# Kernel tuning notes

Hardware: AMD Instinct MI355X
Metric: run time of the kernel (lower is better)

Reference implementation:

```python
import jax, jax.numpy as jnp
import numpy as np

DIM, DIM_KQ, DIM_V, N = 1024, 64, 64, 8192

def setup_inputs() -> dict:
    key = jax.random.key(0)
    kx, kq, kk, kv = jax.random.split(key, 4)
    x = jax.random.normal(kx, (N, DIM), dtype=jnp.float32)
    # original uses torch.rand (uniform [0,1)) for parameter init
    w_q = jax.random.uniform(kq, (DIM, DIM_KQ), dtype=jnp.float32)
    w_k = jax.random.uniform(kk, (DIM, DIM_KQ), dtype=jnp.float32)
    w_v = jax.random.uniform(kv, (DIM, DIM_V), dtype=jnp.float32)
    return {"x": x, "w_q": w_q, "w_k": w_k, "w_v": w_v}

def reference(x, w_q, w_k, w_v):
    q = x @ w_q            # [N, dkq]
    k = x @ w_k            # [N, dkq]
    v = x @ w_v            # [N, dv]
    scale = 1.0 / jnp.sqrt(jnp.asarray(DIM_KQ, dtype=x.dtype))
    att_s = (q @ k.T) * scale           # [N, N]
    att_w = jax.nn.softmax(att_s, axis=-1)
    return att_w @ v                    # [N, dv]
```

## Files before the change

### kernel.cpp

```cpp
#include <hip/hip_runtime.h>
#include <hip/hip_bf16.h>
#include <math.h>

constexpr int N    = 8192;
constexpr int DIM  = 1024;

typedef __attribute__((ext_vector_type(8))) short bf16x8;
typedef __attribute__((ext_vector_type(4))) float f32x4;

__device__ inline unsigned short f2bf(float f) {
    unsigned u = __float_as_uint(f);
    u += 0x7fffu + ((u >> 16) & 1u);
    return (unsigned short)(u >> 16);
}
__device__ inline float bf2f(unsigned short h) {
    return __uint_as_float((unsigned)h << 16);
}
__device__ inline unsigned cvtpk(float a, float b) {
    unsigned r;
    asm("v_cvt_pk_bf16_f32 %0, %1, %2" : "=v"(r) : "v"(a), "v"(b));
    return r;
}
__device__ inline void gload16(const void* gsrc, void* ldst) {
    typedef __attribute__((address_space(1))) const unsigned int GU;
    typedef __attribute__((address_space(3))) unsigned int LU;
    __builtin_amdgcn_global_load_lds((GU*)gsrc, (LU*)ldst, 16, 0, 0);
}

__global__ __launch_bounds__(256) void prep_w_kernel(
    const float* __restrict__ wq, const float* __restrict__ wk,
    const float* __restrict__ wv,
    unsigned short* __restrict__ wthi, unsigned short* __restrict__ wtlo)
{
    int idx = blockIdx.x * 256 + threadIdx.x;
    int c   = idx >> 10;
    int k   = idx & 1023;
    const float* wsrc = (c < 64) ? wq : (c < 128) ? wk : wv;
    float f = wsrc[(size_t)k * 64 + (c & 63)];
    unsigned short h = f2bf(f);
    int pos = c * 1024 + (k & ~63) + ((((k >> 3) & 7) ^ (c & 7)) << 3) + (k & 7);
    wthi[pos] = h;
    wtlo[pos] = f2bf(f - bf2f(h));
}

__global__ __launch_bounds__(256) void proj_kernel(
    const float* __restrict__ x,
    const unsigned short* __restrict__ wthi,
    const unsigned short* __restrict__ wtlo,
    unsigned short* __restrict__ qhi, unsigned short* __restrict__ qlo,
    unsigned short* __restrict__ khi, unsigned short* __restrict__ klo,
    unsigned short* __restrict__ vthi)
{
    __shared__ unsigned short As[2][2][4096];
    __shared__ unsigned short Bs[2][2][3072];

    const int tid  = threadIdx.x;
    const int lane = tid & 63;
    const int w    = tid >> 6;
    const int g16  = lane >> 4;
    const int i16  = lane & 15;
    const int row0 = blockIdx.x * 64;
    const int col0 = blockIdx.y * 48;

    float4 xn[2][4];
    auto loadX = [&](int t, int s) {
#pragma unroll
        for (int i = 0; i < 4; ++i) {
            int f4 = i * 256 + tid;
            xn[s][i] = *reinterpret_cast<const float4*>(
                x + (size_t)(row0 + (f4 >> 4)) * DIM + t * 64 + (f4 & 15) * 4);
        }
    };
    auto stageB = [&](int t, int buf) {
#pragma unroll
        for (int i = 0; i < 3; ++i) {
            int idx = i * 256 + tid;
            int p   = (idx >= 384) ? 1 : 0;
            int li  = idx - p * 384;
            const unsigned short* base = p ? wtlo : wthi;
            const unsigned short* src  = base + (size_t)(col0 + (li >> 3)) * 1024
                                         + t * 64 + (li & 7) * 8;
            gload16(src, (char*)&Bs[buf][p][0] + (size_t)li * 16);
        }
    };
    auto writeA = [&](int buf, int s) {
#pragma unroll
        for (int i = 0; i < 4; ++i) {
            int f4 = i * 256 + tid;
            int r = f4 >> 4, c4 = f4 & 15;
            float4 v = xn[s][i];
            unsigned h01 = cvtpk(v.x, v.y);
            unsigned h23 = cvtpk(v.z, v.w);
            float hx = __uint_as_float(h01 << 16);
            float hy = __uint_as_float(h01 & 0xffff0000u);
            float hz = __uint_as_float(h23 << 16);
            float hw = __uint_as_float(h23 & 0xffff0000u);
            uint2 uh = { h01, h23 };
            uint2 ul = { cvtpk(v.x - hx, v.y - hy), cvtpk(v.z - hz, v.w - hw) };
            int byte = r * 128 + (((c4 >> 1) ^ (r & 7)) << 4) + ((c4 & 1) << 3);
            *reinterpret_cast<uint2*>((char*)&As[buf][0][0] + byte) = uh;
            *reinterpret_cast<uint2*>((char*)&As[buf][1][0] + byte) = ul;
        }
    };

    f32x4 acc[3];
    acc[0] = acc[1] = acc[2] = (f32x4){0.f, 0.f, 0.f, 0.f};

    loadX(0, 0);
    loadX(1, 1);
    stageB(0, 0);
    writeA(0, 0);

    const int arow = w * 16 + i16;
#pragma unroll
    for (int t = 0; t < 16; ++t) {
        const int b = t & 1;
        __syncthreads();
        if (t < 15) stageB(t + 1, b ^ 1);
        if (t < 14) loadX(t + 2, b);
        bf16x8 ah[2], al[2];
#pragma unroll
        for (int kc = 0; kc < 2; ++kc) {
            int off = arow * 128 + ((((kc << 2) | g16) ^ (arow & 7)) << 4);
            ah[kc] = *reinterpret_cast<const bf16x8*>((char*)&As[b][0][0] + off);
            al[kc] = *reinterpret_cast<const bf16x8*>((char*)&As[b][1][0] + off);
        }
#pragma unroll
        for (int ct = 0; ct < 3; ++ct) {
            const int colL = ct * 16 + i16;
#pragma unroll
            for (int kc = 0; kc < 2; ++kc) {
                int off = colL * 128 + ((((kc << 2) | g16) ^ (colL & 7)) << 4);
                bf16x8 bh = *reinterpret_cast<const bf16x8*>((char*)&Bs[b][0][0] + off);
                bf16x8 bl = *reinterpret_cast<const bf16x8*>((char*)&Bs[b][1][0] + off);
                acc[ct] = __builtin_amdgcn_mfma_f32_16x16x32_bf16(ah[kc], bh, acc[ct], 0, 0, 0);
                acc[ct] = __builtin_amdgcn_mfma_f32_16x16x32_bf16(ah[kc], bl, acc[ct], 0, 0, 0);
                acc[ct] = __builtin_amdgcn_mfma_f32_16x16x32_bf16(al[kc], bh, acc[ct], 0, 0, 0);
            }
        }
        if (t < 15) writeA(b ^ 1, b ^ 1);
    }

    const float QSCALE = 0.180336880f;
#pragma unroll
    for (int ct = 0; ct < 3; ++ct) {
        int cglob = col0 + ct * 16 + i16;
        int g = cglob >> 6, c64 = cglob & 63;
#pragma unroll
        for (int rr = 0; rr < 4; ++rr) {
            int row = row0 + w * 16 + 4 * g16 + rr;
            float f = acc[ct][rr];
            if (g == 0) {
                f *= QSCALE;
                unsigned short h = f2bf(f);
                qhi[(size_t)row * 64 + c64] = h;
                qlo[(size_t)row * 64 + c64] = f2bf(f - bf2f(h));
            } else if (g == 1) {
                int ci = c64 ^ ((row & 7) << 3);
                unsigned short h = f2bf(f);
                khi[(size_t)row * 64 + ci] = h;
                klo[(size_t)row * 64 + ci] = f2bf(f - bf2f(h));
            } else {
                int cg  = row >> 3;
                int cgs = (cg & ~7) | ((cg & 7) ^ (c64 & 7));
                vthi[(size_t)c64 * 8192 + cgs * 8 + (row & 7)] = f2bf(f);
            }
        }
    }
}

constexpr int BQ = 128;
constexpr int BK = 64;

__global__ __launch_bounds__(256) void attn_kernel(
    const unsigned short* __restrict__ qhi, const unsigned short* __restrict__ qlo,
    const unsigned short* __restrict__ khi, const unsigned short* __restrict__ klo,
    const unsigned short* __restrict__ vthi,
    float* __restrict__ po, float* __restrict__ pm, float* __restrict__ pl,
    int keys_per_split)
{
    __shared__ __align__(16) unsigned short stage[2][12288];
    __shared__ __align__(16) unsigned short plds[4][2][1024];

    const int tid  = threadIdx.x;
    const int lane = tid & 63;
    const int w    = tid >> 6;
    const int g16  = lane >> 4;
    const int i16  = lane & 15;
    const int qrow0 = blockIdx.x * BQ;
    const int split = blockIdx.y;
    const int key0  = split * keys_per_split;
    const int nt    = keys_per_split / BK;
    const int xorm  = (i16 & 7) << 4;
    const int wbase = i16 * 128;

    bf16x8 qh[2][2], ql[2][2];
#pragma unroll
    for (int s = 0; s < 2; ++s) {
        const size_t qr = (size_t)(qrow0 + w * 32 + s * 16 + i16) * 64;
#pragma unroll
        for (int c = 0; c < 2; ++c) {
            qh[s][c] = *reinterpret_cast<const bf16x8*>(qhi + qr + c * 32 + g16 * 8);
            ql[s][c] = *reinterpret_cast<const bf16x8*>(qlo + qr + c * 32 + g16 * 8);
        }
    }
    bf16x8 ones;
#pragma unroll
    for (int e = 0; e < 8; ++e) ones[e] = (short)0x3F80;

    float m[2] = {-INFINITY, -INFINITY};
    f32x4 o_acc[2][4], o5[2];
#pragma unroll
    for (int s = 0; s < 2; ++s) {
        o5[s] = {0.f, 0.f, 0.f, 0.f};
#pragma unroll
        for (int db = 0; db < 4; ++db) o_acc[s][db] = {0.f, 0.f, 0.f, 0.f};
    }

    auto stageKV = [&](int t, int buf) {
        const int key0t = key0 + t * BK;
#pragma unroll
        for (int u = 0; u < 6; ++u) {
            int row = ((u & 1) << 5) + (tid >> 3);
            int ch  = tid & 7;
            const unsigned short* src;
            if (u < 2)      src = khi  + (size_t)(key0t + row) * 64 + ch * 8;
            else if (u < 4) src = klo  + (size_t)(key0t + row) * 64 + ch * 8;
            else            src = vthi + (size_t)row * 8192 + key0t + ch * 8;
            gload16(src, (char*)&stage[buf][0] + u * 4096 + tid * 16);
        }
    };

    stageKV(0, 0);

    for (int t = 0; t < nt; ++t) {
        const int b = t & 1;
        __syncthreads();
        if (t + 1 < nt) stageKV(t + 1, b ^ 1);
        const char* stg = (const char*)&stage[b][0];

        f32x4 sacc[2][4];
#pragma unroll
        for (int j = 0; j < 4; ++j) {
            sacc[0][j] = {0.f, 0.f, 0.f, 0.f};
            sacc[1][j] = {0.f, 0.f, 0.f, 0.f};
            const int kr = 16 * j + i16;
#pragma unroll
            for (int c = 0; c < 2; ++c) {
                const int byteO = kr * 128 + ((c * 64 + g16 * 16) ^ ((kr & 7) << 4));
                bf16x8 kh = *reinterpret_cast<const bf16x8*>(stg + byteO);
                bf16x8 kl = *reinterpret_cast<const bf16x8*>(stg + byteO + 8192);
#pragma unroll
                for (int s = 0; s < 2; ++s) {
                    sacc[s][j] = __builtin_amdgcn_mfma_f32_16x16x32_bf16(kh, qh[s][c], sacc[s][j], 0, 0, 0);
                    sacc[s][j] = __builtin_amdgcn_mfma_f32_16x16x32_bf16(kh, ql[s][c], sacc[s][j], 0, 0, 0);
                    sacc[s][j] = __builtin_amdgcn_mfma_f32_16x16x32_bf16(kl, qh[s][c], sacc[s][j], 0, 0, 0);
                }
            }
        }

        float aloc[2];
#pragma unroll
        for (int s = 0; s < 2; ++s) {
            float a0 = fmaxf(fmaxf(sacc[s][0][0], sacc[s][0][1]), fmaxf(sacc[s][0][2], sacc[s][0][3]));
            float a1 = fmaxf(fmaxf(sacc[s][1][0], sacc[s][1][1]), fmaxf(sacc[s][1][2], sacc[s][1][3]));
            float a2 = fmaxf(fmaxf(sacc[s][2][0], sacc[s][2][1]), fmaxf(sacc[s][2][2], sacc[s][2][3]));
            float a3 = fmaxf(fmaxf(sacc[s][3][0], sacc[s][3][1]), fmaxf(sacc[s][3][2], sacc[s][3][3]));
            aloc[s] = fmaxf(fmaxf(a0, a1), fmaxf(a2, a3));
        }
        int need = (aloc[0] > m[0] + 8.f) | (aloc[1] > m[1] + 8.f);
        if (__any(need)) {
#pragma unroll
            for (int s = 0; s < 2; ++s) {
                float x2 = fmaxf(aloc[s], __shfl_xor(aloc[s], 16));
                x2 = fmaxf(x2, __shfl_xor(x2, 32));
                float mn   = fmaxf(m[s], x2);
                float corr = exp2f(m[s] - mn);
                m[s] = mn;
                o5[s] *= corr;
#pragma unroll
                for (int db = 0; db < 4; ++db) o_acc[s][db] *= corr;
            }
        }

        bf16x8 pfrag[2][2];
#pragma unroll
        for (int s = 0; s < 2; ++s) {
            char* pb = (char*)&plds[w][s][0];
#pragma unroll
            for (int j = 0; j < 4; ++j) {
                float p0 = exp2f(sacc[s][j][0] - m[s]);
                float p1 = exp2f(sacc[s][j][1] - m[s]);
                float p2 = exp2f(sacc[s][j][2] - m[s]);
                float p3 = exp2f(sacc[s][j][3] - m[s]);
                uint2 pdw = { cvtpk(p0, p1), cvtpk(p2, p3) };
                *reinterpret_cast<uint2*>(pb + wbase + ((32 * j + 8 * g16) ^ xorm)) = pdw;
            }
#pragma unroll
            for (int c = 0; c < 2; ++c)
                pfrag[s][c] = *reinterpret_cast<const bf16x8*>(
                    pb + wbase + ((64 * c + 16 * g16) ^ xorm));
            o5[s] = __builtin_amdgcn_mfma_f32_16x16x32_bf16(ones, pfrag[s][0], o5[s], 0, 0, 0);
            o5[s] = __builtin_amdgcn_mfma_f32_16x16x32_bf16(ones, pfrag[s][1], o5[s], 0, 0, 0);
        }

#pragma unroll
        for (int db = 0; db < 4; ++db) {
            const int vr = 16 * db + i16;
#pragma unroll
            for (int c = 0; c < 2; ++c) {
                const int byteO = 16384 + vr * 128 +
                                  ((c * 64 + g16 * 16) ^ ((vr & 7) << 4));
                bf16x8 vh = *reinterpret_cast<const bf16x8*>(stg + byteO);
#pragma unroll
                for (int s = 0; s < 2; ++s)
                    o_acc[s][db] = __builtin_amdgcn_mfma_f32_16x16x32_bf16(
                                       vh, pfrag[s][c], o_acc[s][db], 0, 0, 0);
            }
        }
    }

#pragma unroll
    for (int s = 0; s < 2; ++s) {
        const size_t prow = (size_t)split * N + qrow0 + w * 32 + s * 16;
#pragma unroll
        for (int db = 0; db < 4; ++db) {
            float4 ov = {o_acc[s][db][0], o_acc[s][db][1],
                         o_acc[s][db][2], o_acc[s][db][3]};
            *reinterpret_cast<float4*>(po + (prow + i16) * 64 + 16 * db + 4 * g16) = ov;
        }
        if (lane < 16) {
            pm[prow + i16] = m[s];
            pl[prow + i16] = o5[s][0];
        }
    }
}

__global__ __launch_bounds__(256) void combine_kernel(
    const float* __restrict__ po,
    const float* __restrict__ pm,
    const float* __restrict__ pl,
    float* __restrict__ out, int ns)
{
    const int tid = threadIdx.x;
    const int row = blockIdx.x * 16 + (tid >> 4);
    const int c4  = tid & 15;

    float M = -INFINITY;
    for (int s = 0; s < ns; ++s)
        M = fmaxf(M, pm[(size_t)s * N + row]);
    float L = 0.f;
    float4 acc = {0.f, 0.f, 0.f, 0.f};
    for (int s = 0; s < ns; ++s) {
        float ws = exp2f(pm[(size_t)s * N + row] - M);
        L += ws * pl[(size_t)s * N + row];
        float4 ov = *reinterpret_cast<const float4*>(
            po + ((size_t)s * N + row) * 64 + c4 * 4);
        acc.x += ws * ov.x; acc.y += ws * ov.y;
        acc.z += ws * ov.z; acc.w += ws * ov.w;
    }
    float inv = 1.f / L;
    float4 res = {acc.x * inv, acc.y * inv, acc.z * inv, acc.w * inv};
    *reinterpret_cast<float4*>(out + (size_t)row * 64 + c4 * 4) = res;
}

extern "C" void kernel_launch(void* const* d_in, const int* in_sizes, int n_in,
                              void* d_out, int out_size, void* d_ws, size_t ws_size,
                              hipStream_t stream)
{
    const float* x  = (const float*)d_in[0];
    const float* wq = (const float*)d_in[1];
    const float* wk = (const float*)d_in[2];
    const float* wv = (const float*)d_in[3];
    float* out = (float*)d_out;

    const size_t PLANE = (size_t)N * 64;
    unsigned short* qhi  = (unsigned short*)d_ws;
    unsigned short* qlo  = qhi + PLANE;
    unsigned short* khi  = qlo + PLANE;
    unsigned short* klo  = khi + PLANE;
    unsigned short* vthi = klo + PLANE;
    const size_t plane_bytes = 5 * PLANE * 2;
    const size_t wt_elems = (size_t)192 * 1024;
    const size_t wt_bytes = 2 * wt_elems * 2;

    int ns = 8;
    while (ns > 1 &&
           plane_bytes + wt_bytes +
           (size_t)ns * ((size_t)N * 64 * 4 + (size_t)N * 8) > ws_size)
        ns >>= 1;

    float* po = (float*)((char*)d_ws + plane_bytes);
    float* pm = po + (size_t)ns * N * 64;
    float* pl = pm + (size_t)ns * N;
    unsigned short* wthi = (unsigned short*)(pl + (size_t)ns * N);
    unsigned short* wtlo = wthi + wt_elems;

    prep_w_kernel<<<768, 256, 0, stream>>>(wq, wk, wv, wthi, wtlo);

    dim3 pgrid(N / 64, 4);
    proj_kernel<<<pgrid, 256, 0, stream>>>(x, wthi, wtlo,
                                           qhi, qlo, khi, klo, vthi);

    dim3 agrid(N / BQ, ns);
    attn_kernel<<<agrid, 256, 0, stream>>>(qhi, qlo, khi, klo, vthi,
                                           po, pm, pl, N / ns);

    combine_kernel<<<N / 16, 256, 0, stream>>>(po, pm, pl, out, ns);
}
```

Before: 84.98 us.

## Use packed f32 ops, incremental staging pointers, and setprio around MFMA blocks

```diff
diff --git a/kernel.cpp b/kernel.cpp
--- a/kernel.cpp
+++ b/kernel.cpp
@@ -7,6 +7,7 @@
 
 typedef __attribute__((ext_vector_type(8))) short bf16x8;
 typedef __attribute__((ext_vector_type(4))) float f32x4;
+typedef __attribute__((ext_vector_type(2))) float f32x2;
 
 __device__ inline unsigned short f2bf(float f) {
     unsigned u = __float_as_uint(f);
@@ -20,6 +21,21 @@
     unsigned r;
     asm("v_cvt_pk_bf16_f32 %0, %1, %2" : "=v"(r) : "v"(a), "v"(b));
     return r;
+}
+__device__ inline f32x2 pkadd(f32x2 a, f32x2 b) {
+    f32x2 r;
+    asm("v_pk_add_f32 %0, %1, %2" : "=v"(r) : "v"(a), "v"(b));
+    return r;
+}
+__device__ inline f32x2 pkmul(f32x2 a, f32x2 b) {
+    f32x2 r;
+    asm("v_pk_mul_f32 %0, %1, %2" : "=v"(r) : "v"(a), "v"(b));
+    return r;
+}
+__device__ inline f32x4 scale4(f32x4 v, f32x2 c) {
+    f32x2 lo = {v[0], v[1]}, hi = {v[2], v[3]};
+    lo = pkmul(lo, c); hi = pkmul(hi, c);
+    return (f32x4){lo[0], lo[1], hi[0], hi[1]};
 }
 __device__ inline void gload16(const void* gsrc, void* ldst) {
     typedef __attribute__((address_space(1))) const unsigned int GU;
@@ -217,28 +233,33 @@
         for (int db = 0; db < 4; ++db) o_acc[s][db] = {0.f, 0.f, 0.f, 0.f};
     }
 
-    auto stageKV = [&](int t, int buf) {
-        const int key0t = key0 + t * BK;
-#pragma unroll
-        for (int u = 0; u < 6; ++u) {
-            int row = ((u & 1) << 5) + (tid >> 3);
-            int ch  = tid & 7;
-            const unsigned short* src;
-            if (u < 2)      src = khi  + (size_t)(key0t + row) * 64 + ch * 8;
-            else if (u < 4) src = klo  + (size_t)(key0t + row) * 64 + ch * 8;
-            else            src = vthi + (size_t)row * 8192 + key0t + ch * 8;
-            gload16(src, (char*)&stage[buf][0] + u * 4096 + tid * 16);
-        }
+    const int srow = tid >> 3, sch = tid & 7;
+    const unsigned short* s0 = khi  + (size_t)(key0 + srow) * 64 + sch * 8;
+    const unsigned short* s1 = khi  + (size_t)(key0 + 32 + srow) * 64 + sch * 8;
+    const unsigned short* s2 = klo  + (size_t)(key0 + srow) * 64 + sch * 8;
+    const unsigned short* s3 = klo  + (size_t)(key0 + 32 + srow) * 64 + sch * 8;
+    const unsigned short* s4 = vthi + (size_t)srow * 8192 + key0 + sch * 8;
+    const unsigned short* s5 = vthi + (size_t)(32 + srow) * 8192 + key0 + sch * 8;
+
+    auto stageKV = [&](int buf) {
+        char* dst = (char*)&stage[buf][0] + tid * 16;
+        gload16(s0, dst);             s0 += 4096;
+        gload16(s1, dst + 4096);      s1 += 4096;
+        gload16(s2, dst + 8192);      s2 += 4096;
+        gload16(s3, dst + 12288);     s3 += 4096;
+        gload16(s4, dst + 16384);     s4 += 64;
+        gload16(s5, dst + 20480);     s5 += 64;
     };
 
-    stageKV(0, 0);
+    stageKV(0);
 
     for (int t = 0; t < nt; ++t) {
         const int b = t & 1;
         __syncthreads();
-        if (t + 1 < nt) stageKV(t + 1, b ^ 1);
+        if (t + 1 < nt) stageKV(b ^ 1);
         const char* stg = (const char*)&stage[b][0];
 
+        __builtin_amdgcn_s_setprio(1);
         f32x4 sacc[2][4];
 #pragma unroll
         for (int j = 0; j < 4; ++j) {
@@ -258,6 +279,7 @@
                 }
             }
         }
+        __builtin_amdgcn_s_setprio(0);
 
         float aloc[2];
 #pragma unroll
@@ -277,9 +299,10 @@
                 float mn   = fmaxf(m[s], x2);
                 float corr = exp2f(m[s] - mn);
                 m[s] = mn;
-                o5[s] *= corr;
-#pragma unroll
-                for (int db = 0; db < 4; ++db) o_acc[s][db] *= corr;
+                f32x2 c2 = {corr, corr};
+                o5[s] = scale4(o5[s], c2);
+#pragma unroll
+                for (int db = 0; db < 4; ++db) o_acc[s][db] = scale4(o_acc[s][db], c2);
             }
         }
 
@@ -287,12 +310,15 @@
 #pragma unroll
         for (int s = 0; s < 2; ++s) {
             char* pb = (char*)&plds[w][s][0];
+            f32x2 nm = {-m[s], -m[s]};
 #pragma unroll
             for (int j = 0; j < 4; ++j) {
-                float p0 = exp2f(sacc[s][j][0] - m[s]);
-                float p1 = exp2f(sacc[s][j][1] - m[s]);
-                float p2 = exp2f(sacc[s][j][2] - m[s]);
-                float p3 = exp2f(sacc[s][j][3] - m[s]);
+                f32x2 d01 = pkadd((f32x2){sacc[s][j][0], sacc[s][j][1]}, nm);
+                f32x2 d23 = pkadd((f32x2){sacc[s][j][2], sacc[s][j][3]}, nm);
+                float p0 = exp2f(d01[0]);
+                float p1 = exp2f(d01[1]);
+                float p2 = exp2f(d23[0]);
+                float p3 = exp2f(d23[1]);
                 uint2 pdw = { cvtpk(p0, p1), cvtpk(p2, p3) };
                 *reinterpret_cast<uint2*>(pb + wbase + ((32 * j + 8 * g16) ^ xorm)) = pdw;
             }
@@ -304,6 +330,7 @@
             o5[s] = __builtin_amdgcn_mfma_f32_16x16x32_bf16(ones, pfrag[s][1], o5[s], 0, 0, 0);
         }
 
+        __builtin_amdgcn_s_setprio(1);
 #pragma unroll
         for (int db = 0; db < 4; ++db) {
             const int vr = 16 * db + i16;
@@ -318,6 +345,7 @@
                                        vh, pfrag[s][c], o_acc[s][db], 0, 0, 0);
             }
         }
+        __builtin_amdgcn_s_setprio(0);
     }
 
 #pragma unroll
```

Result: slower. 86.94 us (+2.3%).
